# Kernel optimization log

Hardware: AMD Instinct MI355X
Metric: run time of the kernel (lower is better)

## Reference

```python
import jax, jax.numpy as jnp
import numpy as np

MAX_SPIKE_TIME = 100.0
TH = 1.0
BIT = 8
K = 3
PAD = 1
OUT_CH = 64


def _unfold3x3(x):
    # torch F.unfold(kernel=3, padding=1, stride=1): output (B, C*9, H*W),
    # feature order channel-major then (kh, kw).
    B, C, H, W = x.shape
    xp = jnp.pad(x, ((0, 0), (0, 0), (PAD, PAD), (PAD, PAD)))
    cols = [xp[:, :, i:i + H, j:j + W] for i in range(K) for j in range(K)]
    p = jnp.stack(cols, axis=2)            # (B, C, 9, H, W)
    return p.reshape(B, C * K * K, H * W)  # (B, C*9, L)


def _weight_quantization(w):
    # tanh -> scale by global abs-max (no grad through alpha) -> round with STE
    w = jnp.tanh(w)
    alpha = jax.lax.stop_gradient(jnp.max(jnp.abs(w)))
    qmax = float(2 ** (BIT - 1) - 1)
    w = jnp.clip(w / alpha, -1.0, 1.0) * qmax
    w_hat = jax.lax.stop_gradient(jnp.round(w) - w) + w
    return w_hat * alpha / qmax


def _t_linear_c(patches, weight):
    # patches: (B, L, F_in); weight: (F_out, F_in)
    sorted_inp = jnp.sort(patches, axis=-1)      # (B, L, F_in)
    indic = jnp.argsort(patches, axis=-1)        # (B, L, F_in)
    wT = weight.T                                # (F_in, F_out)
    w_sorted = wT[indic]                         # (B, L, F_in, F_out)
    wq = _weight_quantization(w_sorted)
    si = sorted_inp[..., None]                   # (B, L, F_in, 1)
    weight_input_mul = si * wq
    weight_sum = jnp.cumsum(wq, axis=-2)
    input_weight_sum = jnp.cumsum(weight_input_mul, axis=-2)
    out_all = input_weight_sum / jnp.clip(weight_sum - TH, 1e-10, 1e10)
    out_spike = jnp.where(weight_sum < TH, MAX_SPIKE_TIME, out_all)
    out_spike = jnp.where(out_spike < si, MAX_SPIKE_TIME, out_spike)
    # causality check against the NEXT sorted input time (1.0 for the last slot)
    next_in = jnp.concatenate([si[..., 1:, :], jnp.ones_like(si[..., :1, :])], axis=-2)
    out_spike = jnp.where(out_spike > next_in, MAX_SPIKE_TIME, out_spike)
    return jnp.min(out_spike, axis=-2)           # (B, L, F_out)


def setup_inputs() -> dict:
    key = jax.random.key(0)
    k1, k2 = jax.random.split(key)
    inp = jax.random.uniform(k1, (4, 16, 32, 32), dtype=jnp.float32)
    in_features = K * K * 16
    weight = jax.random.uniform(k2, (OUT_CH, in_features), dtype=jnp.float32) * (10.0 / in_features)
    return {"inp": inp, "weight": weight}


def reference(inp, weight):
    B, C, H, W = inp.shape
    patches = _unfold3x3(inp).transpose(0, 2, 1)          # (B, L, F_in)
    patches = jnp.where(patches < 0.1, MAX_SPIKE_TIME, patches)
    out = _t_linear_c(patches, weight)                    # (B, L, F_out)
    out = out.transpose(0, 2, 1).reshape(B, OUT_CH, H, W)  # stride=1, pad=1 -> same HW
    return out
```

## Files before the change

### kernel.cpp

```cpp
#include <hip/hip_runtime.h>
#include <math.h>

constexpr int F_IN   = 144;
constexpr int F_OUT  = 64;
constexpr int H_IMG  = 32;
constexpr int W_IMG  = 32;
constexpr int NPIX   = 4 * H_IMG * W_IMG;
constexpr int PPB    = 8;
constexpr int NTHR   = PPB * 64;
#define MAX_SPIKE 100.0f

__device__ __forceinline__ unsigned rl_u32(unsigned v, int j) {
    return (unsigned)__builtin_amdgcn_readlane((int)v, j);
}

__global__ __launch_bounds__(NTHR, 4) void fused_spike_kernel(
    const float* __restrict__ inp,
    const float* __restrict__ w,
    float* __restrict__ out)
{
#pragma clang fp contract(off)
    __shared__ __align__(16) float wql[F_IN * F_OUT];
    __shared__ __align__(16) unsigned long long kr[PPB][F_IN];
    __shared__ float sv[PPB][F_IN + 1];
    __shared__ float red[PPB];

    const int tid  = threadIdx.x;
    const int lane = tid & 63;
    const int wv_i = tid >> 6;
    const int p    = blockIdx.x * PPB + wv_i;
    const int b    = p >> 10;
    const int l    = p & 1023;
    const int h    = l >> 5;
    const int wc   = l & 31;

    float wreg[18];
    float m = 0.f;
#pragma unroll
    for (int t = 0; t < 18; ++t) {
        const int j = tid + 512 * t;
        const int f = j >> 6;
        const int o = j & 63;
        const float x = w[o * F_IN + f];
        wreg[t] = x;
        m = fmaxf(m, fabsf(x));
    }
    for (int s = 32; s > 0; s >>= 1)
        m = fmaxf(m, __shfl_xor(m, s, 64));
    if (lane == 0) red[wv_i] = m;

    float vv[3];
    unsigned long long k64[3];
    unsigned khi[3], klo[3];
#pragma unroll
    for (int mm = 0; mm < 3; ++mm) {
        const int i = lane + 64 * mm;
        float v = MAX_SPIKE;
        if (i < F_IN) {
            const int c  = i / 9;
            const int r  = i - c * 9;
            const int kh = r / 3;
            const int kw = r - kh * 3;
            const int hh = h + kh - 1;
            const int wg = wc + kw - 1;
            float x = 0.f;
            if (hh >= 0 && hh < H_IMG && wg >= 0 && wg < W_IMG)
                x = inp[((b * 16 + c) * H_IMG + hh) * W_IMG + wg];
            v = (x < 0.1f) ? MAX_SPIKE : x;
        }
        vv[mm] = v;
        k64[mm] = ((unsigned long long)__float_as_uint(v) << 8) | (unsigned)i;
        khi[mm] = (unsigned)(k64[mm] >> 32);
        klo[mm] = (unsigned)k64[mm];
    }
    if (lane == 0) sv[wv_i][F_IN] = 1.0f;

    __syncthreads();

    float mw = red[0];
#pragma unroll
    for (int t = 1; t < PPB; ++t) mw = fmaxf(mw, red[t]);
    const float alpha = tanhf(mw);
#pragma unroll
    for (int t = 0; t < 18; ++t) {
        const int j = tid + 512 * t;
        const float tt = tanhf(wreg[t]);
        float x = tt / alpha;
        x = fminf(fmaxf(x, -1.f), 1.f) * 127.f;
        const float r = rintf(x);
        wql[j] = r * alpha / 127.f;
    }

    int vr0 = 0, vr1 = 0, vr2 = 0;
#pragma unroll 8
    for (int j = 0; j < 64; ++j) {
        const unsigned long long sk =
            ((unsigned long long)rl_u32(khi[0], j) << 32) | rl_u32(klo[0], j);
        const int r = (int)(__popcll(__ballot(k64[0] < sk))
                          + __popcll(__ballot(k64[1] < sk))
                          + __popcll(__ballot(k64[2] < sk) & 0xFFFFull));
        vr0 = (lane == j) ? r : vr0;
    }
#pragma unroll 8
    for (int j = 0; j < 64; ++j) {
        const unsigned long long sk =
            ((unsigned long long)rl_u32(khi[1], j) << 32) | rl_u32(klo[1], j);
        const int r = (int)(__popcll(__ballot(k64[0] < sk))
                          + __popcll(__ballot(k64[1] < sk))
                          + __popcll(__ballot(k64[2] < sk) & 0xFFFFull));
        vr1 = (lane == j) ? r : vr1;
    }
#pragma unroll 8
    for (int j = 0; j < 16; ++j) {
        const unsigned long long sk =
            ((unsigned long long)rl_u32(khi[2], j) << 32) | rl_u32(klo[2], j);
        const int r = (int)(__popcll(__ballot(k64[0] < sk))
                          + __popcll(__ballot(k64[1] < sk))
                          + __popcll(__ballot(k64[2] < sk) & 0xFFFFull));
        vr2 = (lane == j) ? r : vr2;
    }

    {
        unsigned* krlo = (unsigned*)&kr[wv_i][0];
        sv[wv_i][vr0] = vv[0];  krlo[2 * vr0] = (unsigned)lane << 6;
        sv[wv_i][vr1] = vv[1];  krlo[2 * vr1] = (unsigned)(lane + 64) << 6;
        if (lane < F_IN - 128) {
            sv[wv_i][vr2] = vv[2];  krlo[2 * vr2] = (unsigned)(lane + 128) << 6;
        }
    }

    {
        unsigned* krhi = (unsigned*)&kr[wv_i][0];
        for (int k = lane; k < F_IN; k += 64)
            krhi[2 * k + 1] = __float_as_uint(sv[wv_i][k + 1]);
    }

    __syncthreads();

    float s   = sv[wv_i][0];
    float ws  = 0.f;
    float iws = 0.f;
    float mn  = MAX_SPIKE;
    bool  done = false;
    const ulonglong2* rec2 = (const ulonglong2*)&kr[wv_i][0];
    for (int k0 = 0; k0 < F_IN; k0 += 8) {
        if (s >= MAX_SPIKE) break;
        const ulonglong2 ra = rec2[(k0 >> 1) + 0];
        const ulonglong2 rb = rec2[(k0 >> 1) + 1];
        const ulonglong2 rc = rec2[(k0 >> 1) + 2];
        const ulonglong2 rd = rec2[(k0 >> 1) + 3];
        const unsigned long long r8[8] = { ra.x, ra.y, rb.x, rb.y,
                                           rc.x, rc.y, rd.x, rd.y };
        float su[8], nx[8], wsu[8], iwsu[8];
#pragma unroll
        for (int u = 0; u < 8; ++u) {
            su[u] = s;
            nx[u] = __uint_as_float((unsigned)(r8[u] >> 32));
            const float wvv = wql[(unsigned)r8[u] + lane];
            ws += wvv;
            const float prod = su[u] * wvv;
            iws += prod;
            wsu[u]  = ws;
            iwsu[u] = iws;
            s = nx[u];
        }
        if (!__all(wsu[7] < 1.0f)) {
#pragma unroll
            for (int u = 0; u < 8; ++u) {
                const float d = fmaxf(wsu[u] - 1.0f, 1e-10f);
                const float q = iwsu[u] / d;
                const bool valid = (wsu[u] >= 1.0f) & (q >= su[u]) & (q <= nx[u]);
                if (valid & !done) { mn = q; done = true; }
            }
            if (__all(done)) break;
        }
    }
    out[(b * F_OUT + lane) * 1024 + l] = mn;
}

extern "C" void kernel_launch(void* const* d_in, const int* in_sizes, int n_in,
                              void* d_out, int out_size, void* d_ws, size_t ws_size,
                              hipStream_t stream) {
    const float* inp = (const float*)d_in[0];
    const float* w   = (const float*)d_in[1];
    float* out = (float*)d_out;

    fused_spike_kernel<<<NPIX / PPB, NTHR, 0, stream>>>(inp, w, out);
}
```

Measured before the change: 91.71 us.

## Precompute quantized weights in a separate kernel and DMA them into LDS

Moves the tanh/abs-max/round weight quantization out of every block into a small prologue kernel that writes transposed quantized weights to workspace. The main kernel then copies the 36 KB table straight into LDS with global_load_lds, so it no longer needs the per-block weight reduction or the tanh work. This removes work that was repeated 512 times, at the price of a second kernel launch and a dependency between the two launches.

Measured after the change: 87.17 us. 1.05x faster.

```diff
diff --git a/kernel.cpp b/kernel.cpp
--- a/kernel.cpp
+++ b/kernel.cpp
@@ -14,16 +14,49 @@
     return (unsigned)__builtin_amdgcn_readlane((int)v, j);
 }
 
-__global__ __launch_bounds__(NTHR, 4) void fused_spike_kernel(
+__global__ __launch_bounds__(256) void quant_fused_kernel(
+    const float* __restrict__ w,
+    float* __restrict__ wqT)
+{
+#pragma clang fp contract(off)
+    __shared__ float wred[4];
+    const int tid = threadIdx.x;
+
+    float m = 0.f;
+    {
+        const float4* w4 = (const float4*)w;
+        for (int i = tid; i < (F_OUT * F_IN) / 4; i += 256) {
+            const float4 v = w4[i];
+            m = fmaxf(m, fmaxf(fmaxf(fabsf(v.x), fabsf(v.y)),
+                               fmaxf(fabsf(v.z), fabsf(v.w))));
+        }
+    }
+    for (int s = 32; s > 0; s >>= 1)
+        m = fmaxf(m, __shfl_xor(m, s, 64));
+    if ((tid & 63) == 0) wred[tid >> 6] = m;
+    __syncthreads();
+    const float mw = fmaxf(fmaxf(wred[0], wred[1]), fmaxf(wred[2], wred[3]));
+    const float alpha = tanhf(mw);
+
+    const int i = blockIdx.x * 256 + tid;
+    const int o = i / F_IN;
+    const int f = i - o * F_IN;
+    const float t = tanhf(w[i]);
+    float x = t / alpha;
+    x = fminf(fmaxf(x, -1.f), 1.f) * 127.f;
+    const float r = rintf(x);
+    wqT[f * F_OUT + o] = r * alpha / 127.f;
+}
+
+__global__ __launch_bounds__(NTHR, 4) void spike_conv_kernel(
     const float* __restrict__ inp,
-    const float* __restrict__ w,
+    const float* __restrict__ wq,
     float* __restrict__ out)
 {
 #pragma clang fp contract(off)
     __shared__ __align__(16) float wql[F_IN * F_OUT];
     __shared__ __align__(16) unsigned long long kr[PPB][F_IN];
     __shared__ float sv[PPB][F_IN + 1];
-    __shared__ float red[PPB];
 
     const int tid  = threadIdx.x;
     const int lane = tid & 63;
@@ -34,20 +67,13 @@
     const int h    = l >> 5;
     const int wc   = l & 31;
 
-    float wreg[18];
-    float m = 0.f;
-#pragma unroll
-    for (int t = 0; t < 18; ++t) {
-        const int j = tid + 512 * t;
-        const int f = j >> 6;
-        const int o = j & 63;
-        const float x = w[o * F_IN + f];
-        wreg[t] = x;
-        m = fmaxf(m, fabsf(x));
-    }
-    for (int s = 32; s > 0; s >>= 1)
-        m = fmaxf(m, __shfl_xor(m, s, 64));
-    if (lane == 0) red[wv_i] = m;
+    for (int c = wv_i; c < 36; c += PPB) {
+        const float* g = wq + c * 256 + lane * 4;
+        __builtin_amdgcn_global_load_lds(
+            (const __attribute__((address_space(1))) void*)g,
+            (__attribute__((address_space(3))) void*)&wql[c * 256],
+            16, 0, 0);
+    }
 
     float vv[3];
     unsigned long long k64[3];
@@ -74,22 +100,6 @@
         klo[mm] = (unsigned)k64[mm];
     }
     if (lane == 0) sv[wv_i][F_IN] = 1.0f;
-
-    __syncthreads();
-
-    float mw = red[0];
-#pragma unroll
-    for (int t = 1; t < PPB; ++t) mw = fmaxf(mw, red[t]);
-    const float alpha = tanhf(mw);
-#pragma unroll
-    for (int t = 0; t < 18; ++t) {
-        const int j = tid + 512 * t;
-        const float tt = tanhf(wreg[t]);
-        float x = tt / alpha;
-        x = fminf(fmaxf(x, -1.f), 1.f) * 127.f;
-        const float r = rintf(x);
-        wql[j] = r * alpha / 127.f;
-    }
 
     int vr0 = 0, vr1 = 0, vr2 = 0;
 #pragma unroll 8
@@ -184,6 +194,8 @@
     const float* inp = (const float*)d_in[0];
     const float* w   = (const float*)d_in[1];
     float* out = (float*)d_out;
-
-    fused_spike_kernel<<<NPIX / PPB, NTHR, 0, stream>>>(inp, w, out);
-}
+    float* wqT = (float*)d_ws;
+
+    quant_fused_kernel<<<36, 256, 0, stream>>>(w, wqT);
+    spike_conv_kernel<<<NPIX / PPB, NTHR, 0, stream>>>(inp, wqT, out);
+}
```
